# Kernel optimization log

Measured on AMD Instinct MI355X. Metric: run time of the kernel, lower is better.

Reference implementation:

```python
import jax, jax.numpy as jnp
import numpy as np

TOP_K = 2


def setup_inputs() -> dict:
    key = jax.random.key(0)
    k0, k1, k2, k3 = jax.random.split(key, 4)
    B, S, H, F, E = 2, 2048, 1024, 4096, 8
    return {
        'hidden_states': jax.random.normal(k0, (B, S, H), jnp.float32) * 0.02,
        'gate_weight': jax.random.normal(k1, (E, H), jnp.float32) * 0.02,        # router Linear(H->E), no bias
        'gate_up_weights': jax.random.normal(k2, (E, 2 * F, H), jnp.float32) * 0.02,  # [w1; w3] stacked
        'down_weights': jax.random.normal(k3, (E, H, F), jnp.float32) * 0.02,    # w2
    }


def reference(hidden_states, gate_weight, gate_up_weights, down_weights):
    B, S, H = hidden_states.shape
    x = hidden_states.reshape(-1, H)                       # [T, H]
    T = x.shape[0]
    E = gate_weight.shape[0]
    F = gate_up_weights.shape[1] // 2

    router_logits = x @ gate_weight.T                      # [T, E]
    routing_weights = jax.nn.softmax(router_logits.astype(jnp.float32), axis=-1)
    topk_w, topk_ids = jax.lax.top_k(routing_weights, TOP_K)  # [T, K]
    topk_w = topk_w / jnp.sum(topk_w, axis=-1, keepdims=True)  # renormalize=True

    # combine[t, e] = routed weight of token t for expert e (0 if not selected)
    combine = jnp.zeros((T, E), dtype=x.dtype).at[
        jnp.arange(T)[:, None], topk_ids
    ].add(topk_w.astype(x.dtype))

    out = jnp.zeros_like(x)
    for e in range(E):  # fixed small expert count; dense-with-zero-weight combine
        w1 = gate_up_weights[e, :F]   # [F, H]
        w3 = gate_up_weights[e, F:]   # [F, H]
        w2 = down_weights[e]          # [H, F]
        h = jax.nn.silu(x @ w1.T) * (x @ w3.T)             # [T, F]
        out = out + combine[:, e:e + 1] * (h @ w2.T)       # [T, H]

    return out.reshape(B, S, H), router_logits
```

## Files before the change

### kernel.cpp

```cpp
#include <hip/hip_runtime.h>
#include <hip/hip_bf16.h>

#define T_TOK 4096
#define HID   1024
#define FDIM  4096
#define NEXP  8

typedef unsigned short u16;
typedef __attribute__((ext_vector_type(8))) __bf16 bf16x8;
typedef __attribute__((ext_vector_type(4))) float  f32x4;

__device__ __forceinline__ u16 f2bf(float f) {
    unsigned u = __float_as_uint(f);
    u += 0x7fffu + ((u >> 16) & 1u);
    return (u16)(u >> 16);
}

__device__ __forceinline__ void gl2lds16(const u16* g, u16* l) {
    __builtin_amdgcn_global_load_lds(
        (const __attribute__((address_space(1))) void*)g,
        (__attribute__((address_space(3))) void*)l, 16, 0, 0);
}

__global__ __launch_bounds__(256) void convert_kernel(
    const float* __restrict__ src, u16* __restrict__ dst, int n4)
{
    const int stride = gridDim.x * blockDim.x;
    for (int i = blockIdx.x * blockDim.x + threadIdx.x; i < n4; i += stride) {
        float4 f = reinterpret_cast<const float4*>(src)[i];
        ushort4 u;
        u.x = f2bf(f.x); u.y = f2bf(f.y); u.z = f2bf(f.z); u.w = f2bf(f.w);
        reinterpret_cast<ushort4*>(dst)[i] = u;
    }
}

__global__ __launch_bounds__(64) void router_kernel(
    const float* __restrict__ x, const float* __restrict__ gw,
    float* __restrict__ out_logits, u16* __restrict__ xbf,
    int* __restrict__ counts, int* __restrict__ tokl, float* __restrict__ wtl)
{
    const int t = blockIdx.x;
    const int lane = threadIdx.x;

    const float4* xr = reinterpret_cast<const float4*>(x + (size_t)t * HID);
    float4 xv[4];
#pragma unroll
    for (int j = 0; j < 4; ++j) xv[j] = xr[lane + 64 * j];

    ushort4* xbr = reinterpret_cast<ushort4*>(xbf + (size_t)t * HID);
#pragma unroll
    for (int j = 0; j < 4; ++j) {
        ushort4 u;
        u.x = f2bf(xv[j].x); u.y = f2bf(xv[j].y);
        u.z = f2bf(xv[j].z); u.w = f2bf(xv[j].w);
        xbr[lane + 64 * j] = u;
    }

    float lg[8];
#pragma unroll
    for (int e = 0; e < 8; ++e) {
        const float4* gr = reinterpret_cast<const float4*>(gw + (size_t)e * HID);
        float s = 0.f;
#pragma unroll
        for (int j = 0; j < 4; ++j) {
            float4 g = gr[lane + 64 * j];
            s += xv[j].x * g.x + xv[j].y * g.y + xv[j].z * g.z + xv[j].w * g.w;
        }
#pragma unroll
        for (int off = 32; off >= 1; off >>= 1) s += __shfl_xor(s, off);
        lg[e] = s;
    }

    if (lane == 0) {
#pragma unroll
        for (int e = 0; e < 8; ++e) out_logits[(size_t)t * 8 + e] = lg[e];
        float m = lg[0];
#pragma unroll
        for (int e = 1; e < 8; ++e) m = fmaxf(m, lg[e]);
        float p[8];
#pragma unroll
        for (int e = 0; e < 8; ++e) p[e] = __expf(lg[e] - m);
        int b0 = 0; float v0 = p[0];
#pragma unroll
        for (int e = 1; e < 8; ++e) { if (p[e] > v0) { v0 = p[e]; b0 = e; } }
        int b1 = -1; float v1 = -1.f;
#pragma unroll
        for (int e = 0; e < 8; ++e) { if (e != b0 && p[e] > v1) { v1 = p[e]; b1 = e; } }
        float inv = 1.f / (v0 + v1);
        int p0 = atomicAdd(&counts[b0], 1);
        tokl[b0 * T_TOK + p0] = t; wtl[b0 * T_TOK + p0] = v0 * inv;
        int p1 = atomicAdd(&counts[b1], 1);
        tokl[b1 * T_TOK + p1] = t; wtl[b1 * T_TOK + p1] = v1 * inv;
    }
}

__global__ void prefix_kernel(const int* __restrict__ counts, int* __restrict__ offs)
{
    if (threadIdx.x == 0 && blockIdx.x == 0) {
        int s = 0;
        for (int e = 0; e < NEXP; ++e) { offs[e] = s; s += counts[e]; }
        offs[NEXP] = s;
    }
}

__global__ __launch_bounds__(256, 2) void gemm1_kernel(
    const u16* __restrict__ xbf, const u16* __restrict__ gupbf,
    u16* __restrict__ h1,
    const int* __restrict__ counts, const int* __restrict__ offs,
    const int* __restrict__ tokl)
{
    const int e = blockIdx.z;
    const int cnt = counts[e];
    const int m0 = blockIdx.y * 128;
    if (m0 >= cnt) return;
    const int n0 = blockIdx.x * 128;
    const int tid = threadIdx.x;
    const int lane = tid & 63;
    const int wid = tid >> 6;
    const int wr = wid >> 1, wc = wid & 1;
    int cntL = cnt - m0; if (cntL > 128) cntL = 128;

    __shared__ alignas(16) u16 As[128 * 64];
    __shared__ alignas(16) u16 B1s[128 * 64];
    __shared__ alignas(16) u16 B3s[128 * 64];
    __shared__ int toks[128];

    if (tid < 128)
        toks[tid] = tokl[e * T_TOK + (tid < cntL ? m0 + tid : m0)];
    __syncthreads();

    const u16* w1 = gupbf + ((size_t)e * 2 * FDIM + n0) * HID;
    const u16* w3 = w1 + (size_t)FDIM * HID;

    const int lr = lane >> 3;
    const int lc = (lane & 7) * 8;
    int rb[4]; size_t aOff[4], bOff[4];
#pragma unroll
    for (int i = 0; i < 4; ++i) {
        rb[i] = (wid * 4 + i) * 8;
        aOff[i] = (size_t)toks[rb[i] + lr] * HID + lc;
        bOff[i] = (size_t)(rb[i] + lr) * HID + lc;
    }

    f32x4 accg[4][4], accu[4][4];
#pragma unroll
    for (int i = 0; i < 4; ++i)
#pragma unroll
        for (int j = 0; j < 4; ++j) {
            accg[i][j] = f32x4{0.f, 0.f, 0.f, 0.f};
            accu[i][j] = f32x4{0.f, 0.f, 0.f, 0.f};
        }

    for (int k0 = 0; k0 < HID; k0 += 64) {
#pragma unroll
        for (int i = 0; i < 4; ++i) {
            gl2lds16(xbf + aOff[i] + k0, &As[rb[i] * 64]);
            gl2lds16(w1 + bOff[i] + k0, &B1s[rb[i] * 64]);
            gl2lds16(w3 + bOff[i] + k0, &B3s[rb[i] * 64]);
        }
        __syncthreads();
#pragma unroll
        for (int kk = 0; kk < 64; kk += 32) {
            bf16x8 a[4], b1[4], b3[4];
            const int co = kk + ((lane >> 4) << 3);
#pragma unroll
            for (int f = 0; f < 4; ++f) {
                int ra = wr * 64 + f * 16 + (lane & 15);
                a[f]  = *reinterpret_cast<const bf16x8*>(&As[ra * 64 + co]);
                int rq = wc * 64 + f * 16 + (lane & 15);
                b1[f] = *reinterpret_cast<const bf16x8*>(&B1s[rq * 64 + co]);
                b3[f] = *reinterpret_cast<const bf16x8*>(&B3s[rq * 64 + co]);
            }
#pragma unroll
            for (int i = 0; i < 4; ++i)
#pragma unroll
                for (int j = 0; j < 4; ++j) {
                    accg[i][j] = __builtin_amdgcn_mfma_f32_16x16x32_bf16(a[i], b1[j], accg[i][j], 0, 0, 0);
                    accu[i][j] = __builtin_amdgcn_mfma_f32_16x16x32_bf16(a[i], b3[j], accu[i][j], 0, 0, 0);
                }
        }
        __syncthreads();
    }

    const size_t hbase = (size_t)offs[e] + m0;
#pragma unroll
    for (int i = 0; i < 4; ++i)
#pragma unroll
        for (int j = 0; j < 4; ++j)
#pragma unroll
            for (int v = 0; v < 4; ++v) {
                int rl = wr * 64 + i * 16 + ((lane >> 4) << 2) + v;
                if (rl < cntL) {
                    float g = accg[i][j][v], u = accu[i][j][v];
                    float h = (g / (1.f + __expf(-g))) * u;
                    int cl = wc * 64 + j * 16 + (lane & 15);
                    h1[(hbase + rl) * FDIM + n0 + cl] = f2bf(h);
                }
            }
}

__global__ __launch_bounds__(256, 2) void gemm2_kernel(
    const u16* __restrict__ h1, const u16* __restrict__ dwbf,
    float* __restrict__ out,
    const int* __restrict__ counts, const int* __restrict__ offs,
    const int* __restrict__ tokl, const float* __restrict__ wtl)
{
    const int e = blockIdx.z;
    const int cnt = counts[e];
    const int m0 = blockIdx.y * 128;
    if (m0 >= cnt) return;
    const int n0 = blockIdx.x * 128;
    const int tid = threadIdx.x;
    const int lane = tid & 63;
    const int wid = tid >> 6;
    const int wr = wid >> 1, wc = wid & 1;
    int cntL = cnt - m0; if (cntL > 128) cntL = 128;

    __shared__ alignas(16) u16 As[128 * 64];
    __shared__ alignas(16) u16 Bs[128 * 64];
    __shared__ int toks[128];
    __shared__ float wts[128];

    if (tid < 128) {
        int r = (tid < cntL ? m0 + tid : m0);
        toks[tid] = tokl[e * T_TOK + r];
        wts[tid]  = wtl[e * T_TOK + r];
    }
    __syncthreads();

    const size_t hrow0 = (size_t)offs[e] + m0;
    const u16* w2 = dwbf + (size_t)e * HID * FDIM + (size_t)n0 * FDIM;

    const int lr = lane >> 3;
    const int lc = (lane & 7) * 8;
    int rb[4]; size_t aOff[4], bOff[4];
#pragma unroll
    for (int i = 0; i < 4; ++i) {
        rb[i] = (wid * 4 + i) * 8;
        int r = rb[i] + lr; if (r >= cntL) r = cntL - 1;
        aOff[i] = (hrow0 + r) * (size_t)FDIM + lc;
        bOff[i] = (size_t)(rb[i] + lr) * FDIM + lc;
    }

    f32x4 acc[4][4];
#pragma unroll
    for (int i = 0; i < 4; ++i)
#pragma unroll
        for (int j = 0; j < 4; ++j) acc[i][j] = f32x4{0.f, 0.f, 0.f, 0.f};

    for (int k0 = 0; k0 < FDIM; k0 += 64) {
#pragma unroll
        for (int i = 0; i < 4; ++i) {
            gl2lds16(h1 + aOff[i] + k0, &As[rb[i] * 64]);
            gl2lds16(w2 + bOff[i] + k0, &Bs[rb[i] * 64]);
        }
        __syncthreads();
#pragma unroll
        for (int kk = 0; kk < 64; kk += 32) {
            bf16x8 a[4], b[4];
            const int co = kk + ((lane >> 4) << 3);
#pragma unroll
            for (int f = 0; f < 4; ++f) {
                int ra = wr * 64 + f * 16 + (lane & 15);
                a[f] = *reinterpret_cast<const bf16x8*>(&As[ra * 64 + co]);
                int rq = wc * 64 + f * 16 + (lane & 15);
                b[f] = *reinterpret_cast<const bf16x8*>(&Bs[rq * 64 + co]);
            }
#pragma unroll
            for (int i = 0; i < 4; ++i)
#pragma unroll
                for (int j = 0; j < 4; ++j)
                    acc[i][j] = __builtin_amdgcn_mfma_f32_16x16x32_bf16(a[i], b[j], acc[i][j], 0, 0, 0);
        }
        __syncthreads();
    }

#pragma unroll
    for (int i = 0; i < 4; ++i)
#pragma unroll
        for (int j = 0; j < 4; ++j)
#pragma unroll
            for (int v = 0; v < 4; ++v) {
                int rl = wr * 64 + i * 16 + ((lane >> 4) << 2) + v;
                if (rl < cntL) {
                    int t = toks[rl];
                    float w = wts[rl];
                    int cl = wc * 64 + j * 16 + (lane & 15);
                    atomicAdd(&out[(size_t)t * HID + n0 + cl], w * acc[i][j][v]);
                }
            }
}

__global__ __launch_bounds__(256, 2) void gemm1_fb_kernel(
    const u16* __restrict__ xbf, const float* __restrict__ gup,
    u16* __restrict__ h1,
    const int* __restrict__ counts, const int* __restrict__ offs,
    const int* __restrict__ tokl)
{
    const int e = blockIdx.z;
    const int cnt = counts[e];
    const int m0 = blockIdx.y * 128;
    if (m0 >= cnt) return;
    const int n0 = blockIdx.x * 128;
    const int tid = threadIdx.x;
    const int lane = tid & 63;
    const int wid = tid >> 6;
    const int wr = wid >> 1, wc = wid & 1;
    int cntL = cnt - m0; if (cntL > 128) cntL = 128;

    __shared__ alignas(16) u16 As[128 * 64];
    __shared__ alignas(16) u16 B1s[128 * 64];
    __shared__ alignas(16) u16 B3s[128 * 64];
    __shared__ int toks[128];

    if (tid < 128)
        toks[tid] = tokl[e * T_TOK + (tid < cntL ? m0 + tid : m0)];
    __syncthreads();

    const float* w1 = gup + ((size_t)e * 2 * FDIM + n0) * HID;
    const float* w3 = w1 + (size_t)FDIM * HID;

    f32x4 accg[4][4], accu[4][4];
#pragma unroll
    for (int i = 0; i < 4; ++i)
#pragma unroll
        for (int j = 0; j < 4; ++j) { accg[i][j] = f32x4{0.f,0.f,0.f,0.f}; accu[i][j] = f32x4{0.f,0.f,0.f,0.f}; }

    for (int k0 = 0; k0 < HID; k0 += 64) {
#pragma unroll
        for (int i = 0; i < 4; ++i) {
            int idx = tid + i * 256;
            int row = idx >> 3, c = idx & 7;
            const u16* src = xbf + (size_t)toks[row] * HID + k0 + c * 8;
            int dst = row * 128 + ((c * 16) ^ ((row & 7) << 4));
            *reinterpret_cast<int4*>(reinterpret_cast<char*>(As) + dst) =
                *reinterpret_cast<const int4*>(src);
        }
#pragma unroll
        for (int i = 0; i < 8; ++i) {
            int idx = tid + i * 256;
            int row = idx >> 4, c4 = idx & 15;
            const float4 f1 = *reinterpret_cast<const float4*>(w1 + (size_t)row * HID + k0 + c4 * 4);
            const float4 f3 = *reinterpret_cast<const float4*>(w3 + (size_t)row * HID + k0 + c4 * 4);
            ushort4 u1; u1.x = f2bf(f1.x); u1.y = f2bf(f1.y); u1.z = f2bf(f1.z); u1.w = f2bf(f1.w);
            ushort4 u3; u3.x = f2bf(f3.x); u3.y = f2bf(f3.y); u3.z = f2bf(f3.z); u3.w = f2bf(f3.w);
            int dst = row * 128 + ((c4 * 8) ^ ((row & 7) << 4));
            *reinterpret_cast<ushort4*>(reinterpret_cast<char*>(B1s) + dst) = u1;
            *reinterpret_cast<ushort4*>(reinterpret_cast<char*>(B3s) + dst) = u3;
        }
        __syncthreads();
#pragma unroll
        for (int kk = 0; kk < 64; kk += 32) {
            bf16x8 a[4], b1[4], b3[4];
            const int colb = (kk + ((lane >> 4) << 3)) * 2;
#pragma unroll
            for (int f = 0; f < 4; ++f) {
                int ra = wr * 64 + f * 16 + (lane & 15);
                a[f] = *reinterpret_cast<const bf16x8*>(reinterpret_cast<const char*>(As) + ra * 128 + (colb ^ ((ra & 7) << 4)));
                int rq = wc * 64 + f * 16 + (lane & 15);
                b1[f] = *reinterpret_cast<const bf16x8*>(reinterpret_cast<const char*>(B1s) + rq * 128 + (colb ^ ((rq & 7) << 4)));
                b3[f] = *reinterpret_cast<const bf16x8*>(reinterpret_cast<const char*>(B3s) + rq * 128 + (colb ^ ((rq & 7) << 4)));
            }
#pragma unroll
            for (int i = 0; i < 4; ++i)
#pragma unroll
                for (int j = 0; j < 4; ++j) {
                    accg[i][j] = __builtin_amdgcn_mfma_f32_16x16x32_bf16(a[i], b1[j], accg[i][j], 0, 0, 0);
                    accu[i][j] = __builtin_amdgcn_mfma_f32_16x16x32_bf16(a[i], b3[j], accu[i][j], 0, 0, 0);
                }
        }
        __syncthreads();
    }

    const size_t hbase = (size_t)offs[e] + m0;
#pragma unroll
    for (int i = 0; i < 4; ++i)
#pragma unroll
        for (int j = 0; j < 4; ++j)
#pragma unroll
            for (int v = 0; v < 4; ++v) {
                int rl = wr * 64 + i * 16 + ((lane >> 4) << 2) + v;
                if (rl < cntL) {
                    float g = accg[i][j][v], u = accu[i][j][v];
                    float h = (g / (1.f + __expf(-g))) * u;
                    int cl = wc * 64 + j * 16 + (lane & 15);
                    h1[(hbase + rl) * FDIM + n0 + cl] = f2bf(h);
                }
            }
}

__global__ __launch_bounds__(256, 2) void gemm2_fb_kernel(
    const u16* __restrict__ h1, const float* __restrict__ dw,
    float* __restrict__ out,
    const int* __restrict__ counts, const int* __restrict__ offs,
    const int* __restrict__ tokl, const float* __restrict__ wtl)
{
    const int e = blockIdx.z;
    const int cnt = counts[e];
    const int m0 = blockIdx.y * 128;
    if (m0 >= cnt) return;
    const int n0 = blockIdx.x * 128;
    const int tid = threadIdx.x;
    const int lane = tid & 63;
    const int wid = tid >> 6;
    const int wr = wid >> 1, wc = wid & 1;
    int cntL = cnt - m0; if (cntL > 128) cntL = 128;

    __shared__ alignas(16) u16 As[128 * 64];
    __shared__ alignas(16) u16 Bs[128 * 64];
    __shared__ int toks[128];
    __shared__ float wts[128];

    if (tid < 128) {
        int r = (tid < cntL ? m0 + tid : m0);
        toks[tid] = tokl[e * T_TOK + r];
        wts[tid]  = wtl[e * T_TOK + r];
    }
    __syncthreads();

    const size_t hrow0 = (size_t)offs[e] + m0;
    const float* w2 = dw + (size_t)e * HID * FDIM + (size_t)n0 * FDIM;

    f32x4 acc[4][4];
#pragma unroll
    for (int i = 0; i < 4; ++i)
#pragma unroll
        for (int j = 0; j < 4; ++j) acc[i][j] = f32x4{0.f,0.f,0.f,0.f};

    for (int k0 = 0; k0 < FDIM; k0 += 64) {
#pragma unroll
        for (int i = 0; i < 4; ++i) {
            int idx = tid + i * 256;
            int row = idx >> 3, c = idx & 7;
            int rr = (row < cntL ? row : 0);
            const u16* src = h1 + (hrow0 + rr) * FDIM + k0 + c * 8;
            int dst = row * 128 + ((c * 16) ^ ((row & 7) << 4));
            *reinterpret_cast<int4*>(reinterpret_cast<char*>(As) + dst) =
                *reinterpret_cast<const int4*>(src);
        }
#pragma unroll
        for (int i = 0; i < 8; ++i) {
            int idx = tid + i * 256;
            int row = idx >> 4, c4 = idx & 15;
            const float4 f = *reinterpret_cast<const float4*>(w2 + (size_t)row * FDIM + k0 + c4 * 4);
            ushort4 u; u.x = f2bf(f.x); u.y = f2bf(f.y); u.z = f2bf(f.z); u.w = f2bf(f.w);
            int dst = row * 128 + ((c4 * 8) ^ ((row & 7) << 4));
            *reinterpret_cast<ushort4*>(reinterpret_cast<char*>(Bs) + dst) = u;
        }
        __syncthreads();
#pragma unroll
        for (int kk = 0; kk < 64; kk += 32) {
            bf16x8 a[4], b[4];
            const int colb = (kk + ((lane >> 4) << 3)) * 2;
#pragma unroll
            for (int f = 0; f < 4; ++f) {
                int ra = wr * 64 + f * 16 + (lane & 15);
                a[f] = *reinterpret_cast<const bf16x8*>(reinterpret_cast<const char*>(As) + ra * 128 + (colb ^ ((ra & 7) << 4)));
                int rq = wc * 64 + f * 16 + (lane & 15);
                b[f] = *reinterpret_cast<const bf16x8*>(reinterpret_cast<const char*>(Bs) + rq * 128 + (colb ^ ((rq & 7) << 4)));
            }
#pragma unroll
            for (int i = 0; i < 4; ++i)
#pragma unroll
                for (int j = 0; j < 4; ++j)
                    acc[i][j] = __builtin_amdgcn_mfma_f32_16x16x32_bf16(a[i], b[j], acc[i][j], 0, 0, 0);
        }
        __syncthreads();
    }

#pragma unroll
    for (int i = 0; i < 4; ++i)
#pragma unroll
        for (int j = 0; j < 4; ++j)
#pragma unroll
            for (int v = 0; v < 4; ++v) {
                int rl = wr * 64 + i * 16 + ((lane >> 4) << 2) + v;
                if (rl < cntL) {
                    int t = toks[rl];
                    float w = wts[rl];
                    int cl = wc * 64 + j * 16 + (lane & 15);
                    atomicAdd(&out[(size_t)t * HID + n0 + cl], w * acc[i][j][v]);
                }
            }
}

extern "C" void kernel_launch(void* const* d_in, const int* in_sizes, int n_in,
                              void* d_out, int out_size, void* d_ws, size_t ws_size,
                              hipStream_t stream)
{
    const float* x   = (const float*)d_in[0];
    const float* gw  = (const float*)d_in[1];
    const float* gup = (const float*)d_in[2];
    const float* dw  = (const float*)d_in[3];
    float* out = (float*)d_out;

    const size_t FAST_NEED = ((size_t)264 << 20) + (512u << 10);
    const bool fast = ws_size >= FAST_NEED;

    char* ws = (char*)d_ws;
    u16* xbf   = (u16*)ws;
    u16* h1    = (u16*)(ws + ((size_t)8 << 20));
    u16* gupbf = (u16*)(ws + ((size_t)72 << 20));
    u16* dwbf  = (u16*)(ws + ((size_t)200 << 20));
    size_t ctrl = fast ? ((size_t)264 << 20) : ((size_t)72 << 20);
    int*   tokl   = (int*)(ws + ctrl);
    float* wtl    = (float*)(ws + ctrl + (128u << 10));
    int*   counts = (int*)(ws + ctrl + (256u << 10));
    int*   offs   = counts + 16;

    hipMemsetAsync(counts, 0, 64, stream);
    hipMemsetAsync(d_out, 0, (size_t)T_TOK * HID * sizeof(float), stream);

    if (fast) {
        convert_kernel<<<2048, 256, 0, stream>>>(gup, gupbf, NEXP * 2 * FDIM * HID / 4);
        convert_kernel<<<2048, 256, 0, stream>>>(dw,  dwbf,  NEXP * HID * FDIM / 4);
    }

    router_kernel<<<T_TOK, 64, 0, stream>>>(x, gw, out + (size_t)T_TOK * HID,
                                            xbf, counts, tokl, wtl);
    prefix_kernel<<<1, 64, 0, stream>>>(counts, offs);

    dim3 g1(FDIM / 128, T_TOK / 128, NEXP);
    dim3 g2(HID / 128, T_TOK / 128, NEXP);
    if (fast) {
        gemm1_kernel<<<g1, 256, 0, stream>>>(xbf, gupbf, h1, counts, offs, tokl);
        gemm2_kernel<<<g2, 256, 0, stream>>>(h1, dwbf, out, counts, offs, tokl, wtl);
    } else {
        gemm1_fb_kernel<<<g1, 256, 0, stream>>>(xbf, gup, h1, counts, offs, tokl);
        gemm2_fb_kernel<<<g2, 256, 0, stream>>>(h1, dw, out, counts, offs, tokl, wtl);
    }
}
```

Baseline: 935.1 us.

## Interleave gate/up weights, shrink gemm1 tile, replace atomic scatter with combine pass

The gate/up conversion now interleaves w1 and w3 rows in 16-row groups, so gemm1 loads a single B tile of 128 rows holding 64 gate and 64 up columns. That halves shared memory and accumulator registers per block and allows three blocks per CU instead of two. gemm2 now writes weighted bf16 rows to a per-slot buffer instead of doing fp32 atomicAdds into the output. A new combine kernel sums each token's two expert rows, which also removes the output memset. The cost is an extra kernel and bf16 rounding of the partial outputs before they are summed.

```diff
diff --git a/kernel.cpp b/kernel.cpp
--- a/kernel.cpp
+++ b/kernel.cpp
@@ -14,6 +14,9 @@
     unsigned u = __float_as_uint(f);
     u += 0x7fffu + ((u >> 16) & 1u);
     return (u16)(u >> 16);
+}
+__device__ __forceinline__ float bf2f(u16 v) {
+    return __uint_as_float((unsigned)v << 16);
 }
 
 __device__ __forceinline__ void gl2lds16(const u16* g, u16* l) {
@@ -34,10 +37,31 @@
     }
 }
 
+__global__ __launch_bounds__(256) void convert_gup_kernel(
+    const float* __restrict__ src, u16* __restrict__ dst)
+{
+    const int total = NEXP * 2 * FDIM * (HID / 4);
+    const int stride = gridDim.x * blockDim.x;
+    for (int i = blockIdx.x * blockDim.x + threadIdx.x; i < total; i += stride) {
+        int c = i & 255;
+        int row = i >> 8;
+        int e = row >> 13;
+        int r = row & 8191;
+        int mat = (r >> 4) & 1;
+        int f = ((r >> 5) << 4) | (r & 15);
+        size_t srcIdx = ((((size_t)e << 13) + ((size_t)mat << 12) + (size_t)f) << 8) + c;
+        float4 v = reinterpret_cast<const float4*>(src)[srcIdx];
+        ushort4 u;
+        u.x = f2bf(v.x); u.y = f2bf(v.y); u.z = f2bf(v.z); u.w = f2bf(v.w);
+        reinterpret_cast<ushort4*>(dst)[i] = u;
+    }
+}
+
 __global__ __launch_bounds__(64) void router_kernel(
     const float* __restrict__ x, const float* __restrict__ gw,
     float* __restrict__ out_logits, u16* __restrict__ xbf,
-    int* __restrict__ counts, int* __restrict__ tokl, float* __restrict__ wtl)
+    int* __restrict__ counts, int* __restrict__ tokl, float* __restrict__ wtl,
+    int4* __restrict__ tokslot)
 {
     const int t = blockIdx.x;
     const int lane = threadIdx.x;
@@ -91,6 +115,7 @@
         tokl[b0 * T_TOK + p0] = t; wtl[b0 * T_TOK + p0] = v0 * inv;
         int p1 = atomicAdd(&counts[b1], 1);
         tokl[b1 * T_TOK + p1] = t; wtl[b1 * T_TOK + p1] = v1 * inv;
+        tokslot[t] = make_int4(b0, p0, b1, p1);
     }
 }
 
@@ -103,11 +128,98 @@
     }
 }
 
-__global__ __launch_bounds__(256, 2) void gemm1_kernel(
+__global__ __launch_bounds__(256, 3) void gemm1_kernel(
     const u16* __restrict__ xbf, const u16* __restrict__ gupbf,
     u16* __restrict__ h1,
     const int* __restrict__ counts, const int* __restrict__ offs,
     const int* __restrict__ tokl)
+{
+    const int e = blockIdx.z;
+    const int cnt = counts[e];
+    const int m0 = blockIdx.y * 128;
+    if (m0 >= cnt) return;
+    const int tid = threadIdx.x;
+    const int lane = tid & 63;
+    const int wid = tid >> 6;
+    const int wr = wid >> 1, wc = wid & 1;
+    int cntL = cnt - m0; if (cntL > 128) cntL = 128;
+
+    __shared__ alignas(16) u16 As[128 * 64];
+    __shared__ alignas(16) u16 Bs[128 * 64];
+    __shared__ int toks[128];
+
+    if (tid < 128)
+        toks[tid] = tokl[e * T_TOK + (tid < cntL ? m0 + tid : m0)];
+    __syncthreads();
+
+    const u16* wB = gupbf + ((size_t)e * 2 * FDIM + (size_t)blockIdx.x * 128) * HID;
+
+    const int lr = lane >> 3;
+    const int lc = (lane & 7) * 8;
+    int rb[4]; size_t aOff[4], bOff[4];
+#pragma unroll
+    for (int i = 0; i < 4; ++i) {
+        rb[i] = (wid * 4 + i) * 8;
+        aOff[i] = (size_t)toks[rb[i] + lr] * HID + lc;
+        bOff[i] = (size_t)(rb[i] + lr) * HID + lc;
+    }
+
+    f32x4 acc[4][4];
+#pragma unroll
+    for (int i = 0; i < 4; ++i)
+#pragma unroll
+        for (int j = 0; j < 4; ++j) acc[i][j] = f32x4{0.f, 0.f, 0.f, 0.f};
+
+    for (int k0 = 0; k0 < HID; k0 += 64) {
+#pragma unroll
+        for (int i = 0; i < 4; ++i) {
+            gl2lds16(xbf + aOff[i] + k0, &As[rb[i] * 64]);
+            gl2lds16(wB + bOff[i] + k0, &Bs[rb[i] * 64]);
+        }
+        __syncthreads();
+#pragma unroll
+        for (int kk = 0; kk < 64; kk += 32) {
+            bf16x8 a[4], b[4];
+            const int co = kk + ((lane >> 4) << 3);
+#pragma unroll
+            for (int f = 0; f < 4; ++f) {
+                int ra = wr * 64 + f * 16 + (lane & 15);
+                a[f] = *reinterpret_cast<const bf16x8*>(&As[ra * 64 + co]);
+                int rq = wc * 64 + f * 16 + (lane & 15);
+                b[f] = *reinterpret_cast<const bf16x8*>(&Bs[rq * 64 + co]);
+            }
+#pragma unroll
+            for (int i = 0; i < 4; ++i)
+#pragma unroll
+                for (int j = 0; j < 4; ++j)
+                    acc[i][j] = __builtin_amdgcn_mfma_f32_16x16x32_bf16(a[i], b[j], acc[i][j], 0, 0, 0);
+        }
+        __syncthreads();
+    }
+
+    const size_t hbase = (size_t)offs[e] + m0;
+    const int fc0 = blockIdx.x * 64 + wc * 32;
+#pragma unroll
+    for (int i = 0; i < 4; ++i)
+#pragma unroll
+        for (int p = 0; p < 2; ++p)
+#pragma unroll
+            for (int v = 0; v < 4; ++v) {
+                int rl = wr * 64 + i * 16 + ((lane >> 4) << 2) + v;
+                if (rl < cntL) {
+                    float g = acc[i][p * 2][v], u = acc[i][p * 2 + 1][v];
+                    float h = (g / (1.f + __expf(-g))) * u;
+                    int col = fc0 + p * 16 + (lane & 15);
+                    h1[(hbase + rl) * FDIM + col] = f2bf(h);
+                }
+            }
+}
+
+__global__ __launch_bounds__(256, 3) void gemm2_kernel(
+    const u16* __restrict__ h1, const u16* __restrict__ dwbf,
+    u16* __restrict__ h2,
+    const int* __restrict__ counts, const int* __restrict__ offs,
+    const int* __restrict__ tokl, const float* __restrict__ wtl)
 {
     const int e = blockIdx.z;
     const int cnt = counts[e];
@@ -121,16 +233,15 @@
     int cntL = cnt - m0; if (cntL > 128) cntL = 128;
 
     __shared__ alignas(16) u16 As[128 * 64];
-    __shared__ alignas(16) u16 B1s[128 * 64];
-    __shared__ alignas(16) u16 B3s[128 * 64];
-    __shared__ int toks[128];
+    __shared__ alignas(16) u16 Bs[128 * 64];
+    __shared__ float wts[128];
 
     if (tid < 128)
-        toks[tid] = tokl[e * T_TOK + (tid < cntL ? m0 + tid : m0)];
+        wts[tid] = wtl[e * T_TOK + (tid < cntL ? m0 + tid : m0)];
     __syncthreads();
 
-    const u16* w1 = gupbf + ((size_t)e * 2 * FDIM + n0) * HID;
-    const u16* w3 = w1 + (size_t)FDIM * HID;
+    const size_t hrow0 = (size_t)offs[e] + m0;
+    const u16* w2 = dwbf + (size_t)e * HID * FDIM + (size_t)n0 * FDIM;
 
     const int lr = lane >> 3;
     const int lc = (lane & 7) * 8;
@@ -138,51 +249,44 @@
 #pragma unroll
     for (int i = 0; i < 4; ++i) {
         rb[i] = (wid * 4 + i) * 8;
-        aOff[i] = (size_t)toks[rb[i] + lr] * HID + lc;
-        bOff[i] = (size_t)(rb[i] + lr) * HID + lc;
-    }
-
-    f32x4 accg[4][4], accu[4][4];
-#pragma unroll
-    for (int i = 0; i < 4; ++i)
-#pragma unroll
-        for (int j = 0; j < 4; ++j) {
-            accg[i][j] = f32x4{0.f, 0.f, 0.f, 0.f};
-            accu[i][j] = f32x4{0.f, 0.f, 0.f, 0.f};
-        }
-
-    for (int k0 = 0; k0 < HID; k0 += 64) {
+        int r = rb[i] + lr; if (r >= cntL) r = cntL - 1;
+        aOff[i] = (hrow0 + r) * (size_t)FDIM + lc;
+        bOff[i] = (size_t)(rb[i] + lr) * FDIM + lc;
+    }
+
+    f32x4 acc[4][4];
+#pragma unroll
+    for (int i = 0; i < 4; ++i)
+#pragma unroll
+        for (int j = 0; j < 4; ++j) acc[i][j] = f32x4{0.f, 0.f, 0.f, 0.f};
+
+    for (int k0 = 0; k0 < FDIM; k0 += 64) {
 #pragma unroll
         for (int i = 0; i < 4; ++i) {
-            gl2lds16(xbf + aOff[i] + k0, &As[rb[i] * 64]);
-            gl2lds16(w1 + bOff[i] + k0, &B1s[rb[i] * 64]);
-            gl2lds16(w3 + bOff[i] + k0, &B3s[rb[i] * 64]);
+            gl2lds16(h1 + aOff[i] + k0, &As[rb[i] * 64]);
+            gl2lds16(w2 + bOff[i] + k0, &Bs[rb[i] * 64]);
         }
         __syncthreads();
 #pragma unroll
         for (int kk = 0; kk < 64; kk += 32) {
-            bf16x8 a[4], b1[4], b3[4];
+            bf16x8 a[4], b[4];
             const int co = kk + ((lane >> 4) << 3);
 #pragma unroll
             for (int f = 0; f < 4; ++f) {
                 int ra = wr * 64 + f * 16 + (lane & 15);
-                a[f]  = *reinterpret_cast<const bf16x8*>(&As[ra * 64 + co]);
+                a[f] = *reinterpret_cast<const bf16x8*>(&As[ra * 64 + co]);
                 int rq = wc * 64 + f * 16 + (lane & 15);
-                b1[f] = *reinterpret_cast<const bf16x8*>(&B1s[rq * 64 + co]);
-                b3[f] = *reinterpret_cast<const bf16x8*>(&B3s[rq * 64 + co]);
+                b[f] = *reinterpret_cast<const bf16x8*>(&Bs[rq * 64 + co]);
             }
 #pragma unroll
             for (int i = 0; i < 4; ++i)
 #pragma unroll
-                for (int j = 0; j < 4; ++j) {
-                    accg[i][j] = __builtin_amdgcn_mfma_f32_16x16x32_bf16(a[i], b1[j], accg[i][j], 0, 0, 0);
-                    accu[i][j] = __builtin_amdgcn_mfma_f32_16x16x32_bf16(a[i], b3[j], accu[i][j], 0, 0, 0);
-                }
-        }
-        __syncthreads();
-    }
-
-    const size_t hbase = (size_t)offs[e] + m0;
+                for (int j = 0; j < 4; ++j)
+                    acc[i][j] = __builtin_amdgcn_mfma_f32_16x16x32_bf16(a[i], b[j], acc[i][j], 0, 0, 0);
+        }
+        __syncthreads();
+    }
+
 #pragma unroll
     for (int i = 0; i < 4; ++i)
 #pragma unroll
@@ -191,19 +295,37 @@
             for (int v = 0; v < 4; ++v) {
                 int rl = wr * 64 + i * 16 + ((lane >> 4) << 2) + v;
                 if (rl < cntL) {
-                    float g = accg[i][j][v], u = accu[i][j][v];
-                    float h = (g / (1.f + __expf(-g))) * u;
+                    float w = wts[rl];
                     int cl = wc * 64 + j * 16 + (lane & 15);
-                    h1[(hbase + rl) * FDIM + n0 + cl] = f2bf(h);
+                    h2[(hrow0 + rl) * HID + n0 + cl] = f2bf(w * acc[i][j][v]);
                 }
             }
 }
 
-__global__ __launch_bounds__(256, 2) void gemm2_kernel(
-    const u16* __restrict__ h1, const u16* __restrict__ dwbf,
-    float* __restrict__ out,
+__global__ __launch_bounds__(256) void combine_kernel(
+    const u16* __restrict__ h2, const int4* __restrict__ tokslot,
+    const int* __restrict__ offs, float* __restrict__ out)
+{
+    const int t = blockIdx.x;
+    const int lane = threadIdx.x;
+    int4 ts = tokslot[t];
+    size_t s0 = (size_t)(offs[ts.x] + ts.y) * HID;
+    size_t s1 = (size_t)(offs[ts.z] + ts.w) * HID;
+    ushort4 a = reinterpret_cast<const ushort4*>(h2 + s0)[lane];
+    ushort4 b = reinterpret_cast<const ushort4*>(h2 + s1)[lane];
+    float4 o;
+    o.x = bf2f(a.x) + bf2f(b.x);
+    o.y = bf2f(a.y) + bf2f(b.y);
+    o.z = bf2f(a.z) + bf2f(b.z);
+    o.w = bf2f(a.w) + bf2f(b.w);
+    reinterpret_cast<float4*>(out + (size_t)t * HID)[lane] = o;
+}
+
+__global__ __launch_bounds__(256, 2) void gemm1_fb_kernel(
+    const u16* __restrict__ xbf, const float* __restrict__ gup,
+    u16* __restrict__ h1,
     const int* __restrict__ counts, const int* __restrict__ offs,
-    const int* __restrict__ tokl, const float* __restrict__ wtl)
+    const int* __restrict__ tokl)
 {
     const int e = blockIdx.z;
     const int cnt = counts[e];
@@ -217,64 +339,70 @@
     int cntL = cnt - m0; if (cntL > 128) cntL = 128;
 
     __shared__ alignas(16) u16 As[128 * 64];
-    __shared__ alignas(16) u16 Bs[128 * 64];
+    __shared__ alignas(16) u16 B1s[128 * 64];
+    __shared__ alignas(16) u16 B3s[128 * 64];
     __shared__ int toks[128];
-    __shared__ float wts[128];
-
-    if (tid < 128) {
-        int r = (tid < cntL ? m0 + tid : m0);
-        toks[tid] = tokl[e * T_TOK + r];
-        wts[tid]  = wtl[e * T_TOK + r];
-    }
+
+    if (tid < 128)
+        toks[tid] = tokl[e * T_TOK + (tid < cntL ? m0 + tid : m0)];
     __syncthreads();
 
-    const size_t hrow0 = (size_t)offs[e] + m0;
-    const u16* w2 = dwbf + (size_t)e * HID * FDIM + (size_t)n0 * FDIM;
-
-    const int lr = lane >> 3;
-    const int lc = (lane & 7) * 8;
-    int rb[4]; size_t aOff[4], bOff[4];
-#pragma unroll
-    for (int i = 0; i < 4; ++i) {
-        rb[i] = (wid * 4 + i) * 8;
-        int r = rb[i] + lr; if (r >= cntL) r = cntL - 1;
-        aOff[i] = (hrow0 + r) * (size_t)FDIM + lc;
-        bOff[i] = (size_t)(rb[i] + lr) * FDIM + lc;
-    }
-
-    f32x4 acc[4][4];
-#pragma unroll
-    for (int i = 0; i < 4; ++i)
-#pragma unroll
-        for (int j = 0; j < 4; ++j) acc[i][j] = f32x4{0.f, 0.f, 0.f, 0.f};
-
-    for (int k0 = 0; k0 < FDIM; k0 += 64) {
+    const float* w1 = gup + ((size_t)e * 2 * FDIM + n0) * HID;
+    const float* w3 = w1 + (size_t)FDIM * HID;
+
+    f32x4 accg[4][4], accu[4][4];
+#pragma unroll
+    for (int i = 0; i < 4; ++i)
+#pragma unroll
+        for (int j = 0; j < 4; ++j) { accg[i][j] = f32x4{0.f,0.f,0.f,0.f}; accu[i][j] = f32x4{0.f,0.f,0.f,0.f}; }
+
+    for (int k0 = 0; k0 < HID; k0 += 64) {
 #pragma unroll
         for (int i = 0; i < 4; ++i) {
-            gl2lds16(h1 + aOff[i] + k0, &As[rb[i] * 64]);
-            gl2lds16(w2 + bOff[i] + k0, &Bs[rb[i] * 64]);
+            int idx = tid + i * 256;
+            int row = idx >> 3, c = idx & 7;
+            const u16* src = xbf + (size_t)toks[row] * HID + k0 + c * 8;
+            int dst = row * 128 + ((c * 16) ^ ((row & 7) << 4));
+            *reinterpret_cast<int4*>(reinterpret_cast<char*>(As) + dst) =
+                *reinterpret_cast<const int4*>(src);
+        }
+#pragma unroll
+        for (int i = 0; i < 8; ++i) {
+            int idx = tid + i * 256;
+            int row = idx >> 4, c4 = idx & 15;
+            const float4 f1 = *reinterpret_cast<const float4*>(w1 + (size_t)row * HID + k0 + c4 * 4);
+            const float4 f3 = *reinterpret_cast<const float4*>(w3 + (size_t)row * HID + k0 + c4 * 4);
+            ushort4 u1; u1.x = f2bf(f1.x); u1.y = f2bf(f1.y); u1.z = f2bf(f1.z); u1.w = f2bf(f1.w);
+            ushort4 u3; u3.x = f2bf(f3.x); u3.y = f2bf(f3.y); u3.z = f2bf(f3.z); u3.w = f2bf(f3.w);
+            int dst = row * 128 + ((c4 * 8) ^ ((row & 7) << 4));
+            *reinterpret_cast<ushort4*>(reinterpret_cast<char*>(B1s) + dst) = u1;
+            *reinterpret_cast<ushort4*>(reinterpret_cast<char*>(B3s) + dst) = u3;
         }
         __syncthreads();
 #pragma unroll
         for (int kk = 0; kk < 64; kk += 32) {
-            bf16x8 a[4], b[4];
-            const int co = kk + ((lane >> 4) << 3);
+            bf16x8 a[4], b1[4], b3[4];
+            const int colb = (kk + ((lane >> 4) << 3)) * 2;
 #pragma unroll
             for (int f = 0; f < 4; ++f) {
                 int ra = wr * 64 + f * 16 + (lane & 15);
-                a[f] = *reinterpret_cast<const bf16x8*>(&As[ra * 64 + co]);
+                a[f] = *reinterpret_cast<const bf16x8*>(reinterpret_cast<const char*>(As) + ra * 128 + (colb ^ ((ra & 7) << 4)));
                 int rq = wc * 64 + f * 16 + (lane & 15);
-                b[f] = *reinterpret_cast<const bf16x8*>(&Bs[rq * 64 + co]);
+                b1[f] = *reinterpret_cast<const bf16x8*>(reinterpret_cast<const char*>(B1s) + rq * 128 + (colb ^ ((rq & 7) << 4)));
+                b3[f] = *reinterpret_cast<const bf16x8*>(reinterpret_cast<const char*>(B3s) + rq * 128 + (colb ^ ((rq & 7) << 4)));
             }
 #pragma unroll
             for (int i = 0; i < 4; ++i)
 #pragma unroll
-                for (int j = 0; j < 4; ++j)
-                    acc[i][j] = __builtin_amdgcn_mfma_f32_16x16x32_bf16(a[i], b[j], acc[i][j], 0, 0, 0);
-        }
-        __syncthreads();
-    }
-
+                for (int j = 0; j < 4; ++j) {
+                    accg[i][j] = __builtin_amdgcn_mfma_f32_16x16x32_bf16(a[i], b1[j], accg[i][j], 0, 0, 0);
+                    accu[i][j] = __builtin_amdgcn_mfma_f32_16x16x32_bf16(a[i], b3[j], accu[i][j], 0, 0, 0);
+                }
+        }
+        __syncthreads();
+    }
+
+    const size_t hbase = (size_t)offs[e] + m0;
 #pragma unroll
     for (int i = 0; i < 4; ++i)
 #pragma unroll
@@ -283,19 +411,19 @@
             for (int v = 0; v < 4; ++v) {
                 int rl = wr * 64 + i * 16 + ((lane >> 4) << 2) + v;
                 if (rl < cntL) {
-                    int t = toks[rl];
-                    float w = wts[rl];
+                    float g = accg[i][j][v], u = accu[i][j][v];
+                    float h = (g / (1.f + __expf(-g))) * u;
                     int cl = wc * 64 + j * 16 + (lane & 15);
-                    atomicAdd(&out[(size_t)t * HID + n0 + cl], w * acc[i][j][v]);
+                    h1[(hbase + rl) * FDIM + n0 + cl] = f2bf(h);
                 }
             }
 }
 
-__global__ __launch_bounds__(256, 2) void gemm1_fb_kernel(
-    const u16* __restrict__ xbf, const float* __restrict__ gup,
-    u16* __restrict__ h1,
+__global__ __launch_bounds__(256, 2) void gemm2_fb_kernel(
+    const u16* __restrict__ h1, const float* __restrict__ dw,
+    float* __restrict__ out,
     const int* __restrict__ counts, const int* __restrict__ offs,
-    const int* __restrict__ tokl)
+    const int* __restrict__ tokl, const float* __restrict__ wtl)
 {
     const int e = blockIdx.z;
     const int cnt = counts[e];
@@ -309,104 +437,6 @@
     int cntL = cnt - m0; if (cntL > 128) cntL = 128;
 
     __shared__ alignas(16) u16 As[128 * 64];
-    __shared__ alignas(16) u16 B1s[128 * 64];
-    __shared__ alignas(16) u16 B3s[128 * 64];
-    __shared__ int toks[128];
-
-    if (tid < 128)
-        toks[tid] = tokl[e * T_TOK + (tid < cntL ? m0 + tid : m0)];
-    __syncthreads();
-
-    const float* w1 = gup + ((size_t)e * 2 * FDIM + n0) * HID;
-    const float* w3 = w1 + (size_t)FDIM * HID;
-
-    f32x4 accg[4][4], accu[4][4];
-#pragma unroll
-    for (int i = 0; i < 4; ++i)
-#pragma unroll
-        for (int j = 0; j < 4; ++j) { accg[i][j] = f32x4{0.f,0.f,0.f,0.f}; accu[i][j] = f32x4{0.f,0.f,0.f,0.f}; }
-
-    for (int k0 = 0; k0 < HID; k0 += 64) {
-#pragma unroll
-        for (int i = 0; i < 4; ++i) {
-            int idx = tid + i * 256;
-            int row = idx >> 3, c = idx & 7;
-            const u16* src = xbf + (size_t)toks[row] * HID + k0 + c * 8;
-            int dst = row * 128 + ((c * 16) ^ ((row & 7) << 4));
-            *reinterpret_cast<int4*>(reinterpret_cast<char*>(As) + dst) =
-                *reinterpret_cast<const int4*>(src);
-        }
-#pragma unroll
-        for (int i = 0; i < 8; ++i) {
-            int idx = tid + i * 256;
-            int row = idx >> 4, c4 = idx & 15;
-            const float4 f1 = *reinterpret_cast<const float4*>(w1 + (size_t)row * HID + k0 + c4 * 4);
-            const float4 f3 = *reinterpret_cast<const float4*>(w3 + (size_t)row * HID + k0 + c4 * 4);
-            ushort4 u1; u1.x = f2bf(f1.x); u1.y = f2bf(f1.y); u1.z = f2bf(f1.z); u1.w = f2bf(f1.w);
-            ushort4 u3; u3.x = f2bf(f3.x); u3.y = f2bf(f3.y); u3.z = f2bf(f3.z); u3.w = f2bf(f3.w);
-            int dst = row * 128 + ((c4 * 8) ^ ((row & 7) << 4));
-            *reinterpret_cast<ushort4*>(reinterpret_cast<char*>(B1s) + dst) = u1;
-            *reinterpret_cast<ushort4*>(reinterpret_cast<char*>(B3s) + dst) = u3;
-        }
-        __syncthreads();
-#pragma unroll
-        for (int kk = 0; kk < 64; kk += 32) {
-            bf16x8 a[4], b1[4], b3[4];
-            const int colb = (kk + ((lane >> 4) << 3)) * 2;
-#pragma unroll
-            for (int f = 0; f < 4; ++f) {
-                int ra = wr * 64 + f * 16 + (lane & 15);
-                a[f] = *reinterpret_cast<const bf16x8*>(reinterpret_cast<const char*>(As) + ra * 128 + (colb ^ ((ra & 7) << 4)));
-                int rq = wc * 64 + f * 16 + (lane & 15);
-                b1[f] = *reinterpret_cast<const bf16x8*>(reinterpret_cast<const char*>(B1s) + rq * 128 + (colb ^ ((rq & 7) << 4)));
-                b3[f] = *reinterpret_cast<const bf16x8*>(reinterpret_cast<const char*>(B3s) + rq * 128 + (colb ^ ((rq & 7) << 4)));
-            }
-#pragma unroll
-            for (int i = 0; i < 4; ++i)
-#pragma unroll
-                for (int j = 0; j < 4; ++j) {
-                    accg[i][j] = __builtin_amdgcn_mfma_f32_16x16x32_bf16(a[i], b1[j], accg[i][j], 0, 0, 0);
-                    accu[i][j] = __builtin_amdgcn_mfma_f32_16x16x32_bf16(a[i], b3[j], accu[i][j], 0, 0, 0);
-                }
-        }
-        __syncthreads();
-    }
-
-    const size_t hbase = (size_t)offs[e] + m0;
-#pragma unroll
-    for (int i = 0; i < 4; ++i)
-#pragma unroll
-        for (int j = 0; j < 4; ++j)
-#pragma unroll
-            for (int v = 0; v < 4; ++v) {
-                int rl = wr * 64 + i * 16 + ((lane >> 4) << 2) + v;
-                if (rl < cntL) {
-                    float g = accg[i][j][v], u = accu[i][j][v];
-                    float h = (g / (1.f + __expf(-g))) * u;
-                    int cl = wc * 64 + j * 16 + (lane & 15);
-                    h1[(hbase + rl) * FDIM + n0 + cl] = f2bf(h);
-                }
-            }
-}
-
-__global__ __launch_bounds__(256, 2) void gemm2_fb_kernel(
-    const u16* __restrict__ h1, const float* __restrict__ dw,
-    float* __restrict__ out,
-    const int* __restrict__ counts, const int* __restrict__ offs,
-    const int* __restrict__ tokl, const float* __restrict__ wtl)
-{
-    const int e = blockIdx.z;
-    const int cnt = counts[e];
-    const int m0 = blockIdx.y * 128;
-    if (m0 >= cnt) return;
-    const int n0 = blockIdx.x * 128;
-    const int tid = threadIdx.x;
-    const int lane = tid & 63;
-    const int wid = tid >> 6;
-    const int wr = wid >> 1, wc = wid & 1;
-    int cntL = cnt - m0; if (cntL > 128) cntL = 128;
-
-    __shared__ alignas(16) u16 As[128 * 64];
     __shared__ alignas(16) u16 Bs[128 * 64];
     __shared__ int toks[128];
     __shared__ float wts[128];
@@ -502,31 +532,37 @@
     u16* h1    = (u16*)(ws + ((size_t)8 << 20));
     u16* gupbf = (u16*)(ws + ((size_t)72 << 20));
     u16* dwbf  = (u16*)(ws + ((size_t)200 << 20));
+    u16* h2    = gupbf;
     size_t ctrl = fast ? ((size_t)264 << 20) : ((size_t)72 << 20);
-    int*   tokl   = (int*)(ws + ctrl);
-    float* wtl    = (float*)(ws + ctrl + (128u << 10));
-    int*   counts = (int*)(ws + ctrl + (256u << 10));
-    int*   offs   = counts + 16;
+    int*   tokl    = (int*)(ws + ctrl);
+    float* wtl     = (float*)(ws + ctrl + (128u << 10));
+    int*   counts  = (int*)(ws + ctrl + (256u << 10));
+    int*   offs    = counts + 16;
+    int4*  tokslot = (int4*)(ws + ctrl + (320u << 10));
 
     hipMemsetAsync(counts, 0, 64, stream);
-    hipMemsetAsync(d_out, 0, (size_t)T_TOK * HID * sizeof(float), stream);
 
     if (fast) {
-        convert_kernel<<<2048, 256, 0, stream>>>(gup, gupbf, NEXP * 2 * FDIM * HID / 4);
-        convert_kernel<<<2048, 256, 0, stream>>>(dw,  dwbf,  NEXP * HID * FDIM / 4);
+        convert_gup_kernel<<<2048, 256, 0, stream>>>(gup, gupbf);
+        convert_kernel<<<2048, 256, 0, stream>>>(dw, dwbf, NEXP * HID * FDIM / 4);
+    } else {
+        hipMemsetAsync(d_out, 0, (size_t)T_TOK * HID * sizeof(float), stream);
     }
 
     router_kernel<<<T_TOK, 64, 0, stream>>>(x, gw, out + (size_t)T_TOK * HID,
-                                            xbf, counts, tokl, wtl);
+                                            xbf, counts, tokl, wtl, tokslot);
     prefix_kernel<<<1, 64, 0, stream>>>(counts, offs);
 
-    dim3 g1(FDIM / 128, T_TOK / 128, NEXP);
-    dim3 g2(HID / 128, T_TOK / 128, NEXP);
     if (fast) {
+        dim3 g1(FDIM / 64, T_TOK / 128, NEXP);
         gemm1_kernel<<<g1, 256, 0, stream>>>(xbf, gupbf, h1, counts, offs, tokl);
-        gemm2_kernel<<<g2, 256, 0, stream>>>(h1, dwbf, out, counts, offs, tokl, wtl);
+        dim3 g2(HID / 128, T_TOK / 128, NEXP);
+        gemm2_kernel<<<g2, 256, 0, stream>>>(h1, dwbf, h2, counts, offs, tokl, wtl);
+        combine_kernel<<<T_TOK, 256, 0, stream>>>(h2, tokslot, offs, out);
     } else {
+        dim3 g1(FDIM / 128, T_TOK / 128, NEXP);
         gemm1_fb_kernel<<<g1, 256, 0, stream>>>(xbf, gup, h1, counts, offs, tokl);
+        dim3 g2(HID / 128, T_TOK / 128, NEXP);
         gemm2_fb_kernel<<<g2, 256, 0, stream>>>(h1, dw, out, counts, offs, tokl, wtl);
     }
 }
```

Result: faster. 890.7 us (-4.7%).
